# Kernel tuning notes

Hardware: AMD Instinct MI355X
Metric: run time of the kernel (lower is better)

## Reference

```python
import math
import jax, jax.numpy as jnp
import numpy as np

B, N, C = 16, 2048, 128
ETA, TAU = 1.0, 1.5


def setup_inputs() -> dict:
    key = jax.random.key(0)
    k1, k2, k3, k4, k5 = jax.random.split(key, 5)
    H_t = jax.random.normal(k1, (B, N, C), dtype=jnp.float32)
    A_stat = jax.random.uniform(k2, (N, N), dtype=jnp.float32)
    M_mask = jax.random.uniform(k3, (N, N), dtype=jnp.float32)
    # nn.Linear(d_model, d_model, bias=False) weights, shape [out, in]
    scale = 1.0 / math.sqrt(C)
    Wq = jax.random.uniform(k4, (C, C), dtype=jnp.float32, minval=-scale, maxval=scale)
    Wk = jax.random.uniform(k5, (C, C), dtype=jnp.float32, minval=-scale, maxval=scale)
    return {"H_t": H_t, "A_stat": A_stat, "M_mask": M_mask, "Wq": Wq, "Wk": Wk}


def reference(H_t, A_stat, M_mask, Wq, Wk):
    c = H_t.shape[-1]
    neg_inf = jnp.array(-jnp.inf, dtype=H_t.dtype)
    # Linear: x @ W.T
    Q = jnp.einsum('bnc,dc->bnd', H_t, Wq)
    K = jnp.einsum('bnc,dc->bnd', H_t, Wk)
    # scaled QK^T, temperature
    logits = jnp.einsum('bnd,bmd->bnm', Q, K) / (math.sqrt(c) * TAU)
    # symmetrize
    logits = 0.5 * (logits + jnp.swapaxes(logits, -1, -2))
    # diagonal mask
    n = logits.shape[-1]
    eye = jnp.eye(n, dtype=bool)
    logits = jnp.where(eye[None, :, :], neg_inf, logits)
    # static-adjacency bias with zeroed diagonal
    A_bias = jnp.where(eye, 0.0, A_stat)
    logits = logits + ETA * A_bias[None, :, :]
    # external mask
    logits = jnp.where((M_mask <= 0)[None, :, :], neg_inf, logits)
    return jax.nn.softmax(logits, axis=-1)
```

## Files before the change

### kernel.cpp

```cpp
#include <hip/hip_runtime.h>
#include <hip/hip_bf16.h>
#include <hip/hip_fp16.h>
#include <math.h>

#define Bn 16
#define Nn 2048
#define Cn 128

typedef __attribute__((ext_vector_type(8))) short bf16x8;
typedef __attribute__((ext_vector_type(4))) float f32x4;

constexpr float SCALE = 0.029462782549439476f;
constexpr float SHIFT = 4.0f;

__device__ __forceinline__ const bf16x8* as_frag(const void* p){
    return reinterpret_cast<const bf16x8*>(p);
}

__device__ __forceinline__ void load16_lds(const void* g, void* l){
    __builtin_amdgcn_global_load_lds(
        (const __attribute__((address_space(1))) void*)g,
        (__attribute__((address_space(3))) void*)l,
        16, 0, 0);
}

__global__ __launch_bounds__(256) void prep_kernel(
    const float* __restrict__ A, const float* __restrict__ M, __half* __restrict__ CB,
    const float* __restrict__ Wq, const float* __restrict__ Wk,
    float* __restrict__ WqT, float* __restrict__ WkT)
{
    size_t idx = (size_t)blockIdx.x * 256 + threadIdx.x;
    int n = (int)(idx >> 11), m = (int)(idx & (Nn-1));
    float a = A[idx];
    float mm = M[idx];
    float v = (mm <= 0.0f || n == m) ? -INFINITY : a;
    CB[idx] = __float2half(v);
    if (blockIdx.x < 64) {
        int widx = (int)idx;
        int d = widx >> 7, c = widx & 127;
        WqT[c*Cn + d] = Wq[widx];
        WkT[c*Cn + d] = Wk[widx];
    }
}

__global__ __launch_bounds__(256) void qk_kernel(
    const float* __restrict__ H, const float* __restrict__ WqT, const float* __restrict__ WkT,
    __hip_bfloat16* __restrict__ Qb, __hip_bfloat16* __restrict__ Kb)
{
    __shared__ __align__(16) float Hs[32*Cn];
    const int t = threadIdx.x;
    const size_t row0 = (size_t)blockIdx.x * 32;
    const float4* src = reinterpret_cast<const float4*>(H + row0*Cn);
    float4* dst = reinterpret_cast<float4*>(Hs);
    #pragma unroll
    for (int i = 0; i < 4; i++) dst[i*256 + t] = src[i*256 + t];
    __syncthreads();
    const int d = t & 127, rh = t >> 7;
    float accq[16], acck[16];
    #pragma unroll
    for (int r = 0; r < 16; r++){ accq[r] = 0.f; acck[r] = 0.f; }
    for (int cb = 0; cb < Cn; cb += 4){
        float wq[4], wk[4];
        #pragma unroll
        for (int j = 0; j < 4; j++){ wq[j] = WqT[(cb+j)*Cn + d]; wk[j] = WkT[(cb+j)*Cn + d]; }
        #pragma unroll
        for (int r = 0; r < 16; r++){
            float4 h = *reinterpret_cast<const float4*>(&Hs[(rh*16+r)*Cn + cb]);
            accq[r] += h.x*wq[0] + h.y*wq[1] + h.z*wq[2] + h.w*wq[3];
            acck[r] += h.x*wk[0] + h.y*wk[1] + h.z*wk[2] + h.w*wk[3];
        }
    }
    #pragma unroll
    for (int r = 0; r < 16; r++){
        size_t row = row0 + rh*16 + r;
        Qb[row*Cn + d] = __float2bfloat16(accq[r]);
        Kb[row*Cn + d] = __float2bfloat16(acck[r]);
    }
}

template<int PASS>
__global__ __launch_bounds__(256) void attn_kernel(
    const __hip_bfloat16* __restrict__ Qb, const __hip_bfloat16* __restrict__ Kb,
    const __half* __restrict__ CB, float* __restrict__ rowsum, float* __restrict__ out)
{
    __shared__ __align__(16) char Ks_s[64*256];
    __shared__ __align__(16) char Qs_s[64*256];
    const int t = threadIdx.x;
    const int wave = t >> 6, lane = t & 63;
    const int q = lane >> 4, lc = lane & 15;
    const int rb = blockIdx.x & 15, ch = blockIdx.x >> 4;
    const int batch = blockIdx.y;
    const int n0 = rb * 128;
    const size_t rbase = (size_t)batch * Nn;

    bf16x8 aQ[2][4], aK[2][4];
    #pragma unroll
    for (int g = 0; g < 2; g++){
        const int nA = n0 + wave*32 + g*16 + lc;
        #pragma unroll
        for (int ks = 0; ks < 4; ks++){
            aQ[g][ks] = *as_frag(Qb + (rbase + nA)*Cn + ks*32 + q*8);
            aK[g][ks] = *as_frag(Kb + (rbase + nA)*Cn + ks*32 + q*8);
        }
    }

    int nout[2][4];
    #pragma unroll
    for (int g = 0; g < 2; g++)
        #pragma unroll
        for (int r = 0; r < 4; r++) nout[g][r] = n0 + wave*32 + g*16 + q*4 + r;

    float rs_inv[2][4];
    if (PASS == 1){
        #pragma unroll
        for (int g = 0; g < 2; g++)
            #pragma unroll
            for (int r = 0; r < 4; r++){
                float s = rowsum[rbase + nout[g][r]] + rowsum[(size_t)Bn*Nn + rbase + nout[g][r]];
                rs_inv[g][r] = 1.0f / s;
            }
    }

    float sumacc[2][4] = {{0.f,0.f,0.f,0.f},{0.f,0.f,0.f,0.f}};

    const int laneoffE = ((lane >> 4) << 8) + ((((lane & 15) ^ (lane >> 4))) << 4);
    int coff[4];
    #pragma unroll
    for (int ks = 0; ks < 4; ks++) coff[ks] = (((4*ks + q) ^ (lc & 7)) << 4);
    const int rowoff = lc * 256;

    const char* gkb = (const char*)Kb;
    const char* gqb = (const char*)Qb;
    const char* gt0 = (wave < 2) ? gkb : gqb;
    void* lt = (wave < 2) ? (void*)Ks_s : (void*)Qs_s;
    const int idx0 = (wave & 1) * 8;

    const int mc0 = ch * (Nn/128);
    for (int mc = mc0; mc < mc0 + Nn/128; mc++){
        __syncthreads();
        {
            const size_t tileoff = (rbase + (size_t)mc*64) * (Cn*2);
            const char* gt = gt0 + tileoff;
            #pragma unroll
            for (int j = 0; j < 8; j++){
                const int idx = idx0 + j;
                const int lo = laneoffE ^ ((j & 1) << 6);
                load16_lds(gt + idx*1024 + lo, (char*)lt + idx*1024);
            }
        }
        __syncthreads();
        #pragma unroll
        for (int mt = 0; mt < 4; mt++){
            const int m0 = mc*64 + mt*16;
            bf16x8 bK[4], bQ[4];
            #pragma unroll
            for (int ks = 0; ks < 4; ks++){
                bK[ks] = *as_frag(Ks_s + mt*4096 + rowoff + coff[ks]);
                bQ[ks] = *as_frag(Qs_s + mt*4096 + rowoff + coff[ks]);
            }
            const int m = m0 + lc;
            #pragma unroll
            for (int g = 0; g < 2; g++){
                f32x4 acc = {0.f,0.f,0.f,0.f};
                #pragma unroll
                for (int ks = 0; ks < 4; ks++){
                    acc = __builtin_amdgcn_mfma_f32_16x16x32_bf16(aQ[g][ks], bK[ks], acc, 0, 0, 0);
                    acc = __builtin_amdgcn_mfma_f32_16x16x32_bf16(aK[g][ks], bQ[ks], acc, 0, 0, 0);
                }
                #pragma unroll
                for (int r = 0; r < 4; r++){
                    const int n = nout[g][r];
                    float logit = fmaf(acc[r], SCALE, __half2float(CB[(size_t)n*Nn + m]));
                    float e = __expf(logit - SHIFT);
                    if (PASS == 0) sumacc[g][r] += e;
                    else out[(rbase + n)*Nn + m] = e * rs_inv[g][r];
                }
            }
        }
    }
    if (PASS == 0){
        float* rs = rowsum + (size_t)ch * (Bn*Nn);
        #pragma unroll
        for (int g = 0; g < 2; g++)
            #pragma unroll
            for (int r = 0; r < 4; r++){
                float s = sumacc[g][r];
                s += __shfl_xor(s, 1);
                s += __shfl_xor(s, 2);
                s += __shfl_xor(s, 4);
                s += __shfl_xor(s, 8);
                if (lc == 0) rs[rbase + nout[g][r]] = s;
            }
    }
}

extern "C" void kernel_launch(void* const* d_in, const int* in_sizes, int n_in,
                              void* d_out, int out_size, void* d_ws, size_t ws_size,
                              hipStream_t stream)
{
    const float* H  = (const float*)d_in[0];
    const float* A  = (const float*)d_in[1];
    const float* M  = (const float*)d_in[2];
    const float* Wq = (const float*)d_in[3];
    const float* Wk = (const float*)d_in[4];
    float* out = (float*)d_out;
    char* ws = (char*)d_ws;
    __hip_bfloat16* Qb = (__hip_bfloat16*)(ws + 0);
    __hip_bfloat16* Kb = (__hip_bfloat16*)(ws + 8388608);
    float* rowsum      = (float*)(ws + 16777216);
    float* WqT         = (float*)(ws + 17825792);
    float* WkT         = (float*)(ws + 17891328);
    __half* CB         = (__half*)(ws + 17956864);

    prep_kernel<<<(Nn*Nn)/256, 256, 0, stream>>>(A, M, CB, Wq, Wk, WqT, WkT);
    qk_kernel<<<(Bn*Nn)/32, 256, 0, stream>>>(H, WqT, WkT, Qb, Kb);
    attn_kernel<0><<<dim3(32, Bn), 256, 0, stream>>>(Qb, Kb, CB, rowsum, out);
    attn_kernel<1><<<dim3(32, Bn), 256, 0, stream>>>(Qb, Kb, CB, rowsum, out);
}
```

Before: 455.6 us.

## Fuse two-pass softmax into one kernel with fp16 scratch of unnormalized exps

Replaces the two attention passes, which recompute QK^T for sums and then for outputs, with one kernel. Each block owns 64 full rows, computes the exps once, writes them as fp16 to a workspace buffer, then normalises them from that buffer into the fp32 output. This removes the duplicated MFMA work and the second read of CB. In exchange it writes and reads back a 128MB intermediate, loses precision by storing exps as fp16, and launches only 512 blocks. It also needs a much larger workspace and falls back to the old path if the workspace is too small.

```diff
diff --git a/kernel.cpp b/kernel.cpp
--- a/kernel.cpp
+++ b/kernel.cpp
@@ -78,8 +78,115 @@
     }
 }
 
+__global__ __launch_bounds__(256) void attn_fused_kernel(
+    const __hip_bfloat16* __restrict__ Qb, const __hip_bfloat16* __restrict__ Kb,
+    const __half* __restrict__ CB, __half* __restrict__ Et, float* __restrict__ out)
+{
+    __shared__ __align__(16) char Ks_s[64*256];
+    __shared__ __align__(16) char Qs_s[64*256];
+    __shared__ float rsinv_s[64];
+    const int t = threadIdx.x;
+    const int wave = t >> 6, lane = t & 63;
+    const int q = lane >> 4, lc = lane & 15;
+    const int batch = blockIdx.y;
+    const int n0 = blockIdx.x * 64;
+    const size_t rbase = (size_t)batch * Nn;
+
+    const int nA = n0 + wave*16 + lc;
+    bf16x8 aQ[4], aK[4];
+    #pragma unroll
+    for (int ks = 0; ks < 4; ks++){
+        aQ[ks] = *as_frag(Qb + (rbase + nA)*Cn + ks*32 + q*8);
+        aK[ks] = *as_frag(Kb + (rbase + nA)*Cn + ks*32 + q*8);
+    }
+
+    int nout[4];
+    #pragma unroll
+    for (int r = 0; r < 4; r++) nout[r] = n0 + wave*16 + q*4 + r;
+
+    float sumacc[4] = {0.f,0.f,0.f,0.f};
+
+    const int laneoffE = ((lane >> 4) << 8) + ((((lane & 15) ^ (lane >> 4))) << 4);
+    int coff[4];
+    #pragma unroll
+    for (int ks = 0; ks < 4; ks++) coff[ks] = (((4*ks + q) ^ (lc & 7)) << 4);
+    const int rowoff = lc * 256;
+
+    const char* gt0 = (wave < 2) ? (const char*)Kb : (const char*)Qb;
+    void* lt = (wave < 2) ? (void*)Ks_s : (void*)Qs_s;
+    const int idx0 = (wave & 1) * 8;
+
+    for (int mc = 0; mc < Nn/64; mc++){
+        __syncthreads();
+        {
+            const size_t tileoff = (rbase + (size_t)mc*64) * (Cn*2);
+            const char* gt = gt0 + tileoff;
+            #pragma unroll
+            for (int j = 0; j < 8; j++){
+                const int idx = idx0 + j;
+                const int lo = laneoffE ^ ((j & 1) << 6);
+                load16_lds(gt + idx*1024 + lo, (char*)lt + idx*1024);
+            }
+        }
+        __syncthreads();
+        #pragma unroll
+        for (int mt = 0; mt < 4; mt++){
+            const int m0 = mc*64 + mt*16;
+            bf16x8 bK[4], bQ[4];
+            #pragma unroll
+            for (int ks = 0; ks < 4; ks++){
+                bK[ks] = *as_frag(Ks_s + mt*4096 + rowoff + coff[ks]);
+                bQ[ks] = *as_frag(Qs_s + mt*4096 + rowoff + coff[ks]);
+            }
+            f32x4 acc = {0.f,0.f,0.f,0.f};
+            #pragma unroll
+            for (int ks = 0; ks < 4; ks++){
+                acc = __builtin_amdgcn_mfma_f32_16x16x32_bf16(aQ[ks], bK[ks], acc, 0, 0, 0);
+                acc = __builtin_amdgcn_mfma_f32_16x16x32_bf16(aK[ks], bQ[ks], acc, 0, 0, 0);
+            }
+            const int m = m0 + lc;
+            #pragma unroll
+            for (int r = 0; r < 4; r++){
+                const int n = nout[r];
+                float logit = fmaf(acc[r], SCALE, __half2float(CB[(size_t)n*Nn + m]));
+                float e = __expf(logit - SHIFT);
+                sumacc[r] += e;
+                Et[(rbase + n)*Nn + m] = __float2half(e);
+            }
+        }
+    }
+    #pragma unroll
+    for (int r = 0; r < 4; r++){
+        float s = sumacc[r];
+        s += __shfl_xor(s, 1);
+        s += __shfl_xor(s, 2);
+        s += __shfl_xor(s, 4);
+        s += __shfl_xor(s, 8);
+        if (lc == 0) rsinv_s[wave*16 + q*4 + r] = 1.0f / s;
+    }
+    __syncthreads();
+
+    const __half* srcT = Et + (rbase + n0) * Nn;
+    float* dstT = out + (rbase + n0) * Nn;
+    #pragma unroll 2
+    for (int r = 0; r < 64; r++){
+        const float rs = rsinv_s[r];
+        const __half2* s2 = reinterpret_cast<const __half2*>(srcT + (size_t)r * Nn);
+        float4* d4 = reinterpret_cast<float4*>(dstT + (size_t)r * Nn);
+        #pragma unroll
+        for (int h = 0; h < 2; h++){
+            const int c4 = h*256 + t;
+            __half2 a = s2[c4*2];
+            __half2 b = s2[c4*2 + 1];
+            float2 fa = __half22float2(a), fb = __half22float2(b);
+            float4 o; o.x = fa.x*rs; o.y = fa.y*rs; o.z = fb.x*rs; o.w = fb.y*rs;
+            d4[c4] = o;
+        }
+    }
+}
+
 template<int PASS>
-__global__ __launch_bounds__(256) void attn_kernel(
+__global__ __launch_bounds__(256) void attn2_kernel(
     const __hip_bfloat16* __restrict__ Qb, const __hip_bfloat16* __restrict__ Kb,
     const __half* __restrict__ CB, float* __restrict__ rowsum, float* __restrict__ out)
 {
@@ -103,7 +210,6 @@
             aK[g][ks] = *as_frag(Kb + (rbase + nA)*Cn + ks*32 + q*8);
         }
     }
-
     int nout[2][4];
     #pragma unroll
     for (int g = 0; g < 2; g++)
@@ -120,7 +226,6 @@
                 rs_inv[g][r] = 1.0f / s;
             }
     }
-
     float sumacc[2][4] = {{0.f,0.f,0.f,0.f},{0.f,0.f,0.f,0.f}};
 
     const int laneoffE = ((lane >> 4) << 8) + ((((lane & 15) ^ (lane >> 4))) << 4);
@@ -129,9 +234,7 @@
     for (int ks = 0; ks < 4; ks++) coff[ks] = (((4*ks + q) ^ (lc & 7)) << 4);
     const int rowoff = lc * 256;
 
-    const char* gkb = (const char*)Kb;
-    const char* gqb = (const char*)Qb;
-    const char* gt0 = (wave < 2) ? gkb : gqb;
+    const char* gt0 = (wave < 2) ? (const char*)Kb : (const char*)Qb;
     void* lt = (wave < 2) ? (void*)Ks_s : (void*)Qs_s;
     const int idx0 = (wave & 1) * 8;
 
@@ -207,13 +310,20 @@
     char* ws = (char*)d_ws;
     __hip_bfloat16* Qb = (__hip_bfloat16*)(ws + 0);
     __hip_bfloat16* Kb = (__hip_bfloat16*)(ws + 8388608);
-    float* rowsum      = (float*)(ws + 16777216);
-    float* WqT         = (float*)(ws + 17825792);
-    float* WkT         = (float*)(ws + 17891328);
-    __half* CB         = (__half*)(ws + 17956864);
+    float* WqT         = (float*)(ws + 16777216);
+    float* WkT         = (float*)(ws + 16842752);
+    __half* CB         = (__half*)(ws + 16908288);
 
     prep_kernel<<<(Nn*Nn)/256, 256, 0, stream>>>(A, M, CB, Wq, Wk, WqT, WkT);
     qk_kernel<<<(Bn*Nn)/32, 256, 0, stream>>>(H, WqT, WkT, Qb, Kb);
-    attn_kernel<0><<<dim3(32, Bn), 256, 0, stream>>>(Qb, Kb, CB, rowsum, out);
-    attn_kernel<1><<<dim3(32, Bn), 256, 0, stream>>>(Qb, Kb, CB, rowsum, out);
-}
+
+    const size_t NEEDED = 25296896ull + (size_t)Bn*Nn*Nn*2;
+    if (ws_size >= NEEDED){
+        __half* Et = (__half*)(ws + 25296896);
+        attn_fused_kernel<<<dim3(Nn/64, Bn), 256, 0, stream>>>(Qb, Kb, CB, Et, out);
+    } else {
+        float* rowsum = (float*)(ws + 25296896);
+        attn2_kernel<0><<<dim3(32, Bn), 256, 0, stream>>>(Qb, Kb, CB, rowsum, out);
+        attn2_kernel<1><<<dim3(32, Bn), 256, 0, stream>>>(Qb, Kb, CB, rowsum, out);
+    }
+}
```

Result: slower. 480.7 us (+5.5%).
